# Performance work log

Measured on AMD Instinct MI355X. Metric: run time of the kernel, lower is better.

The kernel has to match this reference:

```python
import jax, jax.numpy as jnp
import numpy as np

N = 262144
DIM = 256
NUM_HEADS = 4
HEAD_DIM = DIM // NUM_HEADS
B = 4096
SCALE = HEAD_DIM ** (-0.5)
EPS = 1e-8


def setup_inputs() -> dict:
    key = jax.random.key(0)
    ks = jax.random.split(key, 7)
    x = jax.random.normal(ks[0], (N, DIM), dtype=jnp.float32)
    batch = jnp.sort(jax.random.randint(ks[1], (N,), 0, B)).astype(jnp.int64)
    query = jax.random.normal(ks[2], (NUM_HEADS, HEAD_DIM), dtype=jnp.float32)
    # nn.Linear default init scale ~ 1/sqrt(dim); keep exp() well-behaved
    key_w = jax.random.normal(ks[3], (DIM, DIM), dtype=jnp.float32) / np.sqrt(DIM)
    key_b = jax.random.normal(ks[4], (DIM,), dtype=jnp.float32) * 0.01
    value_w = jax.random.normal(ks[5], (DIM, DIM), dtype=jnp.float32) / np.sqrt(DIM)
    value_b = jax.random.normal(ks[6], (DIM,), dtype=jnp.float32) * 0.01
    return {"x": x, "batch": batch, "query": query, "key_w": key_w,
            "key_b": key_b, "value_w": value_w, "value_b": value_b}


def reference(x, batch, query, key_w, key_b, value_w, value_b):
    # k, v: [N, H, Hd]  (torch Linear: x @ W.T + b)
    k = (x @ key_w.T + key_b).reshape(N, NUM_HEADS, HEAD_DIM)
    v = (x @ value_w.T + value_b).reshape(N, NUM_HEADS, HEAD_DIM)
    # attn: [N, H] -- dot of learned per-head query with each node's key
    attn = jnp.einsum('hd,nhd->nh', query, k) * SCALE
    attn_exp = jnp.exp(attn)  # faithful: no max-subtraction in original
    # segment softmax denominator gathered back to nodes: [N, H]
    attn_sum = jax.ops.segment_sum(attn_exp, batch, num_segments=B)[batch]
    attn_norm = attn_exp / (attn_sum + EPS)
    # weighted values scatter-added per segment: [B, H, Hd]
    weighted = attn_norm[:, :, None] * v
    pooled = jax.ops.segment_sum(weighted, batch, num_segments=B)
    return pooled.reshape(B, DIM)
```

## Files before the change

### kernel.cpp

```cpp
#include <hip/hip_runtime.h>


constexpr int DIM = 256;
constexpr int NH  = 4;
constexpr int HD  = 64;
constexpr float SCL  = 0.125f;
constexpr float EPSV = 1e-8f;

constexpr int WS_QW   = 0;
constexpr int WS_QB   = 1024;
constexpr int WS_OFFS = 1088;
constexpr int WS_VWT  = 8192;

template<int CTRL>
__device__ __forceinline__ float dpp_ror_add(float v){
  int r = __builtin_amdgcn_update_dpp(0, __float_as_int(v), CTRL, 0xF, 0xF, false);
  return v + __int_as_float(r);
}
__device__ __forceinline__ float red32(float v){
  v = dpp_ror_add<0x121>(v);
  v = dpp_ror_add<0x122>(v);
  v = dpp_ror_add<0x124>(v);
  v = dpp_ror_add<0x128>(v);
  int r = __builtin_amdgcn_ds_swizzle(__float_as_int(v), 0x401F);
  return v + __int_as_float(r);
}

__global__ void prep_seg(const float* __restrict__ query,
                         const float* __restrict__ key_w,
                         const float* __restrict__ key_b,
                         const float* __restrict__ value_w,
                         const int* __restrict__ batch32,
                         float* __restrict__ ws,
                         int* __restrict__ offs,
                         int N, int B, int do_vwt){
  const int bid = blockIdx.x, tid = threadIdx.x;
  if (bid < 64){
    if (do_vwt){
      float4 v = *(const float4*)(value_w + (size_t)tid*DIM + 4*bid);
      ((float4*)(ws + WS_VWT))[bid*256 + tid] = v;
    }
  } else if (bid < 68){
    int t = (bid - 64)*256 + tid;
    int h = t >> 8, j = t & 255;
    float acc = 0.f;
    #pragma unroll 8
    for (int d = 0; d < HD; ++d)
      acc += query[h*HD+d] * key_w[(size_t)(h*HD+d)*DIM + j];
    ws[WS_QW + t] = acc;
    if (j == 0){
      float bb = 0.f;
      for (int d = 0; d < HD; ++d)
        bb += query[h*HD+d] * key_b[h*HD+d];
      ws[WS_QB + h] = bb;
    }
  } else {
    int i = (bid - 68)*256 + tid;
    if (i >= N) return;
    const bool is64 = (batch32[N-1] == 0);
    int v  = is64 ? batch32[2*i] : batch32[i];
    int vp = (i == 0) ? -1 : (is64 ? batch32[2*(i-1)] : batch32[i-1]);
    for (int b = vp + 1; b <= v; ++b) offs[b] = i;
    if (i == N-1)
      for (int b = v + 1; b <= B; ++b) offs[b] = N;
  }
}

__global__ __launch_bounds__(256, 4)
void attn_fused2(const float* __restrict__ x,
                 const int* __restrict__ offs,
                 const float* __restrict__ ws,
                 const float* __restrict__ value_b,
                 float* __restrict__ out){
  __shared__ __align__(16) float S_all[4][NH*DIM];
  __shared__ __align__(16) float Sfin[NH*DIM];
  __shared__ float sums_all[4][NH];
  __shared__ float invs[NH], wsums[NH];

  const int b   = blockIdx.x;
  const int tid = threadIdx.x;
  const int s = offs[b], e = offs[b+1];

  const int wave = tid >> 6, lane = tid & 63;
  const int half = lane >> 5, sl = lane & 31;
  const int sigma = wave * 2 + half;

  float qwr[NH][8];
  #pragma unroll
  for (int h = 0; h < NH; ++h){
    float4 a = *(const float4*)(ws + WS_QW + h*DIM + 4*sl);
    float4 c = *(const float4*)(ws + WS_QW + h*DIM + 128 + 4*sl);
    qwr[h][0]=a.x; qwr[h][1]=a.y; qwr[h][2]=a.z; qwr[h][3]=a.w;
    qwr[h][4]=c.x; qwr[h][5]=c.y; qwr[h][6]=c.z; qwr[h][7]=c.w;
  }
  float qb[NH];
  #pragma unroll
  for (int h = 0; h < NH; ++h) qb[h] = ws[WS_QB + h];

  float Sacc[NH][8];
  #pragma unroll
  for (int h = 0; h < NH; ++h)
    #pragma unroll
    for (int c = 0; c < 8; ++c) Sacc[h][c] = 0.f;
  float se[NH] = {0.f, 0.f, 0.f, 0.f};

  const float4* xr4 = (const float4*)x;
  const float4 Z = make_float4(0.f, 0.f, 0.f, 0.f);

  int n0 = s + sigma*2;
  bool v0 = n0 < e;
  bool v1 = n0 + 1 < e;
  float4 a0=Z, b0=Z, a1=Z, b1=Z;
  if (v0){ a0 = xr4[(size_t)n0*64 + sl];     b0 = xr4[(size_t)n0*64 + 32 + sl]; }
  if (v1){ a1 = xr4[(size_t)(n0+1)*64 + sl]; b1 = xr4[(size_t)(n0+1)*64 + 32 + sl]; }

  while (v0){
    const int nn = n0 + 16;
    const bool w0 = nn < e;
    const bool w1 = nn + 1 < e;
    float4 c0=Z, d0=Z, c1=Z, d1=Z;
    if (w0){ c0 = xr4[(size_t)nn*64 + sl];     d0 = xr4[(size_t)nn*64 + 32 + sl]; }
    if (w1){ c1 = xr4[(size_t)(nn+1)*64 + sl]; d1 = xr4[(size_t)(nn+1)*64 + 32 + sl]; }

    float xv0[8] = {a0.x,a0.y,a0.z,a0.w,b0.x,b0.y,b0.z,b0.w};
    float xv1[8] = {a1.x,a1.y,a1.z,a1.w,b1.x,b1.y,b1.z,b1.w};

    float p0[NH], p1[NH];
    #pragma unroll
    for (int h = 0; h < NH; ++h){
      float s0 = 0.f, s1 = 0.f;
      #pragma unroll
      for (int c = 0; c < 8; ++c){ s0 += qwr[h][c]*xv0[c]; s1 += qwr[h][c]*xv1[c]; }
      p0[h] = s0; p1[h] = s1;
    }
    #pragma unroll
    for (int h = 0; h < NH; ++h){
      p0[h] = red32(p0[h]);
      p1[h] = red32(p1[h]);
    }
    const float g1 = v1 ? 1.f : 0.f;
    #pragma unroll
    for (int h = 0; h < NH; ++h){
      float e0 = __expf((p0[h] + qb[h]) * SCL);
      float e1 = __expf((p1[h] + qb[h]) * SCL) * g1;
      se[h] += e0 + e1;
      #pragma unroll
      for (int c = 0; c < 8; ++c)
        Sacc[h][c] += e0*xv0[c] + e1*xv1[c];
    }
    n0 = nn; v0 = w0; v1 = w1;
    a0 = c0; b0 = d0; a1 = c1; b1 = d1;
  }

  #pragma unroll
  for (int h = 0; h < NH; ++h){
    se[h] += __shfl_xor(se[h], 32, 64);
    #pragma unroll
    for (int c = 0; c < 8; ++c) Sacc[h][c] += __shfl_xor(Sacc[h][c], 32, 64);
  }
  if (half == 0){
    #pragma unroll
    for (int h = 0; h < NH; ++h){
      float4 lo = make_float4(Sacc[h][0], Sacc[h][1], Sacc[h][2], Sacc[h][3]);
      float4 hi = make_float4(Sacc[h][4], Sacc[h][5], Sacc[h][6], Sacc[h][7]);
      *(float4*)&S_all[wave][h*DIM + 4*sl]       = lo;
      *(float4*)&S_all[wave][h*DIM + 128 + 4*sl] = hi;
    }
    if (sl == 0){
      #pragma unroll
      for (int h = 0; h < NH; ++h) sums_all[wave][h] = se[h];
    }
  }
  __syncthreads();

  #pragma unroll
  for (int k = 0; k < 4; ++k){
    const int idx = tid + k*256;
    Sfin[idx] = S_all[0][idx] + S_all[1][idx] + S_all[2][idx] + S_all[3][idx];
  }
  if (tid < NH){
    float tot = sums_all[0][tid] + sums_all[1][tid]
              + sums_all[2][tid] + sums_all[3][tid];
    float inv = 1.f / (tot + EPSV);
    invs[tid]  = inv;
    wsums[tid] = tot * inv;
  }
  __syncthreads();

  const int t = tid, h = t >> 6;
  const float4* vwt4 = (const float4*)(ws + WS_VWT);
  const float4* sp   = (const float4*)&Sfin[h*256];
  float acc = 0.f;
  #pragma unroll 8
  for (int jj = 0; jj < 64; ++jj){
    const float4 w4 = vwt4[jj*256 + t];
    const float4 s4 = sp[jj];
    acc += w4.x*s4.x + w4.y*s4.y + w4.z*s4.z + w4.w*s4.w;
  }
  out[(size_t)b*256 + t] = acc * invs[h] + wsums[h] * value_b[t];
}

__global__ __launch_bounds__(512, 4)
void attn_pool_fused(const float* __restrict__ x,
                     const int* __restrict__ offs,
                     const float* __restrict__ ws,
                     const float* __restrict__ value_w,
                     const float* __restrict__ value_b,
                     float* __restrict__ out){
  __shared__ __align__(16) float lds[8192 + 32 + 1024 + 512 + 8];
  float* S_all    = lds;
  float* sums_all = lds + 8192;

  const int b   = blockIdx.x;
  const int tid = threadIdx.x;
  const int seg_start = offs[b];
  const int seg_end   = offs[b+1];

  const int wave = tid >> 6, lane = tid & 63;
  const int half = lane >> 5, sl = lane & 31;
  const int sigma = wave * 2 + half;

  float qwr[NH][8];
  #pragma unroll
  for (int h = 0; h < NH; ++h){
    float4 a = *(const float4*)(ws + WS_QW + h*DIM + 4*sl);
    float4 c = *(const float4*)(ws + WS_QW + h*DIM + 128 + 4*sl);
    qwr[h][0]=a.x; qwr[h][1]=a.y; qwr[h][2]=a.z; qwr[h][3]=a.w;
    qwr[h][4]=c.x; qwr[h][5]=c.y; qwr[h][6]=c.z; qwr[h][7]=c.w;
  }
  float qb[NH];
  #pragma unroll
  for (int h = 0; h < NH; ++h) qb[h] = ws[WS_QB + h];

  float Sacc[NH][8];
  #pragma unroll
  for (int h = 0; h < NH; ++h)
    #pragma unroll
    for (int c = 0; c < 8; ++c) Sacc[h][c] = 0.f;
  float se[NH] = {0.f, 0.f, 0.f, 0.f};

  const float4* xr4 = (const float4*)x;
  const float4 Z = make_float4(0.f,0.f,0.f,0.f);

  int n0 = seg_start + sigma*2;
  bool v0 = n0 < seg_end;
  bool v1 = n0 + 1 < seg_end;
  float4 a0=Z, b0=Z, a1=Z, b1=Z;
  if (v0){ a0 = xr4[(size_t)n0*64 + sl];     b0 = xr4[(size_t)n0*64 + 32 + sl]; }
  if (v1){ a1 = xr4[(size_t)(n0+1)*64 + sl]; b1 = xr4[(size_t)(n0+1)*64 + 32 + sl]; }

  while (v0){
    const int nn = n0 + 32;
    const bool w0 = nn < seg_end;
    const bool w1 = nn + 1 < seg_end;
    float4 c0=Z, d0=Z, c1=Z, d1=Z;
    if (w0){ c0 = xr4[(size_t)nn*64 + sl];     d0 = xr4[(size_t)nn*64 + 32 + sl]; }
    if (w1){ c1 = xr4[(size_t)(nn+1)*64 + sl]; d1 = xr4[(size_t)(nn+1)*64 + 32 + sl]; }

    float xv0[8] = {a0.x,a0.y,a0.z,a0.w,b0.x,b0.y,b0.z,b0.w};
    float xv1[8] = {a1.x,a1.y,a1.z,a1.w,b1.x,b1.y,b1.z,b1.w};

    float p0[NH], p1[NH];
    #pragma unroll
    for (int h = 0; h < NH; ++h){
      float s0 = 0.f, s1 = 0.f;
      #pragma unroll
      for (int c = 0; c < 8; ++c){ s0 += qwr[h][c]*xv0[c]; s1 += qwr[h][c]*xv1[c]; }
      p0[h] = s0; p1[h] = s1;
    }
    #pragma unroll
    for (int m = 1; m < 32; m <<= 1){
      #pragma unroll
      for (int h = 0; h < NH; ++h){
        p0[h] += __shfl_xor(p0[h], m, 64);
        p1[h] += __shfl_xor(p1[h], m, 64);
      }
    }
    const float g1 = v1 ? 1.f : 0.f;
    #pragma unroll
    for (int h = 0; h < NH; ++h){
      float e0 = __expf((p0[h] + qb[h]) * SCL);
      float e1 = __expf((p1[h] + qb[h]) * SCL) * g1;
      se[h] += e0 + e1;
      #pragma unroll
      for (int c = 0; c < 8; ++c)
        Sacc[h][c] += e0*xv0[c] + e1*xv1[c];
    }
    n0 = nn; v0 = w0; v1 = w1;
    a0 = c0; b0 = d0; a1 = c1; b1 = d1;
  }

  #pragma unroll
  for (int h = 0; h < NH; ++h){
    se[h] += __shfl_xor(se[h], 32, 64);
    #pragma unroll
    for (int c = 0; c < 8; ++c) Sacc[h][c] += __shfl_xor(Sacc[h][c], 32, 64);
  }
  if (half == 0){
    #pragma unroll
    for (int h = 0; h < NH; ++h){
      float4 lo = make_float4(Sacc[h][0], Sacc[h][1], Sacc[h][2], Sacc[h][3]);
      float4 hi = make_float4(Sacc[h][4], Sacc[h][5], Sacc[h][6], Sacc[h][7]);
      *(float4*)&S_all[wave*1024 + h*DIM + 4*sl]       = lo;
      *(float4*)&S_all[wave*1024 + h*DIM + 128 + 4*sl] = hi;
    }
    if (sl == 0){
      #pragma unroll
      for (int h = 0; h < NH; ++h) sums_all[wave*4 + h] = se[h];
    }
  }
  __syncthreads();

  float* Sfin  = lds + 8224;
  float* invs  = lds + 9760;
  float* wsums = invs + 4;
  #pragma unroll
  for (int k = 0; k < 2; ++k){
    const int idx = tid + k*512;
    float sv = 0.f;
    #pragma unroll
    for (int w = 0; w < 8; ++w) sv += S_all[w*1024 + idx];
    Sfin[idx] = sv;
  }
  if (tid < NH){
    float tot = 0.f;
    #pragma unroll
    for (int w = 0; w < 8; ++w) tot += sums_all[w*4 + tid];
    float inv = 1.f / (tot + EPSV);
    invs[tid] = inv; wsums[tid] = tot * inv;
  }
  __syncthreads();

  float* ep2 = lds + 9248;
  const int t = tid & 255, part = tid >> 8;
  const int h2 = t >> 6;
  const float4* vrow = (const float4*)(value_w + (size_t)t * DIM) + part*32;
  const float4* sp   = (const float4*)&Sfin[h2*256] + part*32;
  float acc = 0.f;
  #pragma unroll
  for (int q = 0; q < 32; ++q){
    float4 r = vrow[q];
    float4 sv = sp[q];
    acc += r.x*sv.x + r.y*sv.y + r.z*sv.z + r.w*sv.w;
  }
  ep2[part*256 + t] = acc;
  __syncthreads();
  if (part == 0)
    out[(size_t)b * DIM + t] = (ep2[t] + ep2[256 + t]) * invs[h2] + wsums[h2] * value_b[t];
}

extern "C" void kernel_launch(void* const* d_in, const int* in_sizes, int n_in,
                              void* d_out, int out_size, void* d_ws, size_t ws_size,
                              hipStream_t stream){
  const float* x       = (const float*)d_in[0];
  const int*   batch   = (const int*)d_in[1];
  const float* query   = (const float*)d_in[2];
  const float* key_w   = (const float*)d_in[3];
  const float* key_b   = (const float*)d_in[4];
  const float* value_w = (const float*)d_in[5];
  const float* value_b = (const float*)d_in[6];
  float* ws  = (float*)d_ws;
  float* out = (float*)d_out;

  const int N = in_sizes[1];
  const int B = out_size / DIM;

  int* offs = (int*)(ws + WS_OFFS);

  const size_t need_vwt = ((size_t)WS_VWT + 65536) * sizeof(float);
  const int do_vwt = (ws_size >= need_vwt) ? 1 : 0;

  const int seg_blocks = (N + 255) / 256;
  prep_seg<<<68 + seg_blocks, 256, 0, stream>>>(query, key_w, key_b, value_w,
                                                batch, ws, offs, N, B, do_vwt);
  if (do_vwt)
    attn_fused2<<<B, 256, 0, stream>>>(x, offs, ws, value_b, out);
  else
    attn_pool_fused<<<B, 512, 0, stream>>>(x, offs, ws, value_w, value_b, out);
}
```

Measured before the change: 393.4 us.

## Stage segment rows through double-buffered LDS tiles with block-cooperative loads

The main attention-pooling kernel now loads each 16-row tile of x cooperatively into a double-buffered shared-memory tile, using fully coalesced float4 loads clamped at the segment end. While the current tile is being computed, the next tile is prefetched into registers. The shared buffer is reused afterwards for the per-wave partial sums. Occupancy is lowered to 3 blocks per CU, and every tile now costs a block-wide barrier, which adds sync overhead compared with the old per-wave register prefetch.

```diff
diff --git a/kernel.cpp b/kernel.cpp
--- a/kernel.cpp
+++ b/kernel.cpp
@@ -66,20 +66,20 @@
   }
 }
 
-__global__ __launch_bounds__(256, 4)
-void attn_fused2(const float* __restrict__ x,
-                 const int* __restrict__ offs,
-                 const float* __restrict__ ws,
-                 const float* __restrict__ value_b,
-                 float* __restrict__ out){
-  __shared__ __align__(16) float S_all[4][NH*DIM];
-  __shared__ __align__(16) float Sfin[NH*DIM];
+__global__ __launch_bounds__(256, 3)
+void attn_tile(const float* __restrict__ x,
+               const int* __restrict__ offs,
+               const float* __restrict__ ws,
+               const float* __restrict__ value_b,
+               float* __restrict__ out){
+  __shared__ __align__(16) float lds[8192];
   __shared__ float sums_all[4][NH];
   __shared__ float invs[NH], wsums[NH];
 
   const int b   = blockIdx.x;
   const int tid = threadIdx.x;
   const int s = offs[b], e = offs[b+1];
+  const int len = e - s;
 
   const int wave = tid >> 6, lane = tid & 63;
   const int half = lane >> 5, sl = lane & 31;
@@ -105,52 +105,83 @@
   float se[NH] = {0.f, 0.f, 0.f, 0.f};
 
   const float4* xr4 = (const float4*)x;
-  const float4 Z = make_float4(0.f, 0.f, 0.f, 0.f);
-
-  int n0 = s + sigma*2;
-  bool v0 = n0 < e;
-  bool v1 = n0 + 1 < e;
-  float4 a0=Z, b0=Z, a1=Z, b1=Z;
-  if (v0){ a0 = xr4[(size_t)n0*64 + sl];     b0 = xr4[(size_t)n0*64 + 32 + sl]; }
-  if (v1){ a1 = xr4[(size_t)(n0+1)*64 + sl]; b1 = xr4[(size_t)(n0+1)*64 + 32 + sl]; }
-
-  while (v0){
-    const int nn = n0 + 16;
-    const bool w0 = nn < e;
-    const bool w1 = nn + 1 < e;
-    float4 c0=Z, d0=Z, c1=Z, d1=Z;
-    if (w0){ c0 = xr4[(size_t)nn*64 + sl];     d0 = xr4[(size_t)nn*64 + 32 + sl]; }
-    if (w1){ c1 = xr4[(size_t)(nn+1)*64 + sl]; d1 = xr4[(size_t)(nn+1)*64 + 32 + sl]; }
-
-    float xv0[8] = {a0.x,a0.y,a0.z,a0.w,b0.x,b0.y,b0.z,b0.w};
-    float xv1[8] = {a1.x,a1.y,a1.z,a1.w,b1.x,b1.y,b1.z,b1.w};
-
-    float p0[NH], p1[NH];
-    #pragma unroll
-    for (int h = 0; h < NH; ++h){
-      float s0 = 0.f, s1 = 0.f;
-      #pragma unroll
-      for (int c = 0; c < 8; ++c){ s0 += qwr[h][c]*xv0[c]; s1 += qwr[h][c]*xv1[c]; }
-      p0[h] = s0; p1[h] = s1;
-    }
-    #pragma unroll
-    for (int h = 0; h < NH; ++h){
-      p0[h] = red32(p0[h]);
-      p1[h] = red32(p1[h]);
-    }
-    const float g1 = v1 ? 1.f : 0.f;
-    #pragma unroll
-    for (int h = 0; h < NH; ++h){
-      float e0 = __expf((p0[h] + qb[h]) * SCL);
-      float e1 = __expf((p1[h] + qb[h]) * SCL) * g1;
-      se[h] += e0 + e1;
-      #pragma unroll
-      for (int c = 0; c < 8; ++c)
-        Sacc[h][c] += e0*xv0[c] + e1*xv1[c];
-    }
-    n0 = nn; v0 = w0; v1 = w1;
-    a0 = c0; b0 = d0; a1 = c1; b1 = d1;
-  }
+  float4* lbuf4 = (float4*)lds;
+
+  if (len > 0){
+    const int ntiles = (len + 15) >> 4;
+    const long gmax = (long)e * 64 - 1;
+
+    {
+      float4 r0[4];
+      #pragma unroll
+      for (int j = 0; j < 4; ++j){
+        long gi = (long)s*64 + tid + j*256;
+        gi = gi < gmax ? gi : gmax;
+        r0[j] = xr4[gi];
+      }
+      #pragma unroll
+      for (int j = 0; j < 4; ++j) lbuf4[tid + j*256] = r0[j];
+    }
+    __syncthreads();
+
+    int cur = 0;
+    for (int k = 0; k < ntiles; ++k){
+      float4 rn[4];
+      const bool more = (k + 1 < ntiles);
+      if (more){
+        const long tb = (long)(s + (k+1)*16) * 64;
+        #pragma unroll
+        for (int j = 0; j < 4; ++j){
+          long gi = tb + tid + j*256;
+          gi = gi < gmax ? gi : gmax;
+          rn[j] = xr4[gi];
+        }
+      }
+
+      const float* base = lds + cur*4096;
+      const int gr0 = s + k*16 + 2*sigma;
+      float4 a0 = *(const float4*)(base + (2*sigma)*256 + 4*sl);
+      float4 b0 = *(const float4*)(base + (2*sigma)*256 + 128 + 4*sl);
+      float4 a1 = *(const float4*)(base + (2*sigma+1)*256 + 4*sl);
+      float4 b1 = *(const float4*)(base + (2*sigma+1)*256 + 128 + 4*sl);
+
+      float xv0[8] = {a0.x,a0.y,a0.z,a0.w,b0.x,b0.y,b0.z,b0.w};
+      float xv1[8] = {a1.x,a1.y,a1.z,a1.w,b1.x,b1.y,b1.z,b1.w};
+
+      float p0[NH], p1[NH];
+      #pragma unroll
+      for (int h = 0; h < NH; ++h){
+        float s0 = 0.f, s1 = 0.f;
+        #pragma unroll
+        for (int c = 0; c < 8; ++c){ s0 += qwr[h][c]*xv0[c]; s1 += qwr[h][c]*xv1[c]; }
+        p0[h] = s0; p1[h] = s1;
+      }
+      #pragma unroll
+      for (int h = 0; h < NH; ++h){
+        p0[h] = red32(p0[h]);
+        p1[h] = red32(p1[h]);
+      }
+      const float g0 = (gr0     < e) ? 1.f : 0.f;
+      const float g1 = (gr0 + 1 < e) ? 1.f : 0.f;
+      #pragma unroll
+      for (int h = 0; h < NH; ++h){
+        float e0 = __expf((p0[h] + qb[h]) * SCL) * g0;
+        float e1 = __expf((p1[h] + qb[h]) * SCL) * g1;
+        se[h] += e0 + e1;
+        #pragma unroll
+        for (int c = 0; c < 8; ++c)
+          Sacc[h][c] += e0*xv0[c] + e1*xv1[c];
+      }
+
+      if (more){
+        #pragma unroll
+        for (int j = 0; j < 4; ++j) lbuf4[(cur^1)*1024 + tid + j*256] = rn[j];
+      }
+      __syncthreads();
+      cur ^= 1;
+    }
+  }
+  __syncthreads();
 
   #pragma unroll
   for (int h = 0; h < NH; ++h){
@@ -158,13 +189,15 @@
     #pragma unroll
     for (int c = 0; c < 8; ++c) Sacc[h][c] += __shfl_xor(Sacc[h][c], 32, 64);
   }
+  float* S_all = lds;
+  float* Sfin  = lds + 4096;
   if (half == 0){
     #pragma unroll
     for (int h = 0; h < NH; ++h){
       float4 lo = make_float4(Sacc[h][0], Sacc[h][1], Sacc[h][2], Sacc[h][3]);
       float4 hi = make_float4(Sacc[h][4], Sacc[h][5], Sacc[h][6], Sacc[h][7]);
-      *(float4*)&S_all[wave][h*DIM + 4*sl]       = lo;
-      *(float4*)&S_all[wave][h*DIM + 128 + 4*sl] = hi;
+      *(float4*)&S_all[wave*1024 + h*DIM + 4*sl]       = lo;
+      *(float4*)&S_all[wave*1024 + h*DIM + 128 + 4*sl] = hi;
     }
     if (sl == 0){
       #pragma unroll
@@ -176,7 +209,8 @@
   #pragma unroll
   for (int k = 0; k < 4; ++k){
     const int idx = tid + k*256;
-    Sfin[idx] = S_all[0][idx] + S_all[1][idx] + S_all[2][idx] + S_all[3][idx];
+    Sfin[idx] = S_all[0*1024 + idx] + S_all[1*1024 + idx]
+              + S_all[2*1024 + idx] + S_all[3*1024 + idx];
   }
   if (tid < NH){
     float tot = sums_all[0][tid] + sums_all[1][tid]
@@ -374,7 +408,7 @@
   prep_seg<<<68 + seg_blocks, 256, 0, stream>>>(query, key_w, key_b, value_w,
                                                 batch, ws, offs, N, B, do_vwt);
   if (do_vwt)
-    attn_fused2<<<B, 256, 0, stream>>>(x, offs, ws, value_b, out);
+    attn_tile<<<B, 256, 0, stream>>>(x, offs, ws, value_b, out);
   else
     attn_pool_fused<<<B, 512, 0, stream>>>(x, offs, ws, value_w, value_b, out);
 }
```

New measurement: 442.6 us. 12.5% more time.

## Process eight segments per block to amortize value-weight projection loads

Applied to the files above, without the earlier changes.

Each block now handles eight consecutive segments with 512 threads. It accumulates per-segment weighted x sums in LDS, then runs one shared pass over the transposed value weights that serves all eight segments, splitting the 64-step reduction across two thread halves. This is meant to cut the repeated global reads of the 256 KB value-weight matrix per segment and the per-block launch overhead. In exchange the grid shrinks from 4096 to 512 blocks, there are many more __syncthreads, and segments within a block are processed serially, which can hurt load balance and occupancy.

```diff
diff --git a/kernel.cpp b/kernel.cpp
--- a/kernel.cpp
+++ b/kernel.cpp
@@ -4,6 +4,7 @@
 constexpr int DIM = 256;
 constexpr int NH  = 4;
 constexpr int HD  = 64;
+constexpr int G   = 8;
 constexpr float SCL  = 0.125f;
 constexpr float EPSV = 1e-8f;
 
@@ -66,21 +67,19 @@
   }
 }
 
-__global__ __launch_bounds__(256, 4)
-void attn_fused2(const float* __restrict__ x,
-                 const int* __restrict__ offs,
-                 const float* __restrict__ ws,
-                 const float* __restrict__ value_b,
-                 float* __restrict__ out){
-  __shared__ __align__(16) float S_all[4][NH*DIM];
-  __shared__ __align__(16) float Sfin[NH*DIM];
-  __shared__ float sums_all[4][NH];
-  __shared__ float invs[NH], wsums[NH];
-
-  const int b   = blockIdx.x;
+__global__ __launch_bounds__(512, 4)
+void attn_g8(const float* __restrict__ x,
+             const int* __restrict__ offs,
+             const float* __restrict__ ws,
+             const float* __restrict__ value_b,
+             float* __restrict__ out){
+  __shared__ __align__(16) float S_all[8][1024];
+  __shared__ __align__(16) float Sfin[G][1024];
+  __shared__ float sums_all[8][NH];
+  __shared__ float invs[G][NH], wsums[G][NH];
+
+  const int b0  = blockIdx.x * G;
   const int tid = threadIdx.x;
-  const int s = offs[b], e = offs[b+1];
-
   const int wave = tid >> 6, lane = tid & 63;
   const int half = lane >> 5, sl = lane & 31;
   const int sigma = wave * 2 + half;
@@ -97,107 +96,131 @@
   #pragma unroll
   for (int h = 0; h < NH; ++h) qb[h] = ws[WS_QB + h];
 
-  float Sacc[NH][8];
-  #pragma unroll
-  for (int h = 0; h < NH; ++h)
-    #pragma unroll
-    for (int c = 0; c < 8; ++c) Sacc[h][c] = 0.f;
-  float se[NH] = {0.f, 0.f, 0.f, 0.f};
-
   const float4* xr4 = (const float4*)x;
   const float4 Z = make_float4(0.f, 0.f, 0.f, 0.f);
 
-  int n0 = s + sigma*2;
-  bool v0 = n0 < e;
-  bool v1 = n0 + 1 < e;
-  float4 a0=Z, b0=Z, a1=Z, b1=Z;
-  if (v0){ a0 = xr4[(size_t)n0*64 + sl];     b0 = xr4[(size_t)n0*64 + 32 + sl]; }
-  if (v1){ a1 = xr4[(size_t)(n0+1)*64 + sl]; b1 = xr4[(size_t)(n0+1)*64 + 32 + sl]; }
-
-  while (v0){
-    const int nn = n0 + 16;
-    const bool w0 = nn < e;
-    const bool w1 = nn + 1 < e;
-    float4 c0=Z, d0=Z, c1=Z, d1=Z;
-    if (w0){ c0 = xr4[(size_t)nn*64 + sl];     d0 = xr4[(size_t)nn*64 + 32 + sl]; }
-    if (w1){ c1 = xr4[(size_t)(nn+1)*64 + sl]; d1 = xr4[(size_t)(nn+1)*64 + 32 + sl]; }
-
-    float xv0[8] = {a0.x,a0.y,a0.z,a0.w,b0.x,b0.y,b0.z,b0.w};
-    float xv1[8] = {a1.x,a1.y,a1.z,a1.w,b1.x,b1.y,b1.z,b1.w};
-
-    float p0[NH], p1[NH];
+  for (int g = 0; g < G; ++g){
+    const int s = offs[b0 + g], e = offs[b0 + g + 1];
+
+    float Sacc[NH][8];
+    #pragma unroll
+    for (int h = 0; h < NH; ++h)
+      #pragma unroll
+      for (int c = 0; c < 8; ++c) Sacc[h][c] = 0.f;
+    float se[NH] = {0.f, 0.f, 0.f, 0.f};
+
+    int n0 = s + sigma*2;
+    bool v0 = n0 < e;
+    bool v1 = n0 + 1 < e;
+    float4 la0=Z, lb0=Z, la1=Z, lb1=Z;
+    if (v0){ la0 = xr4[(size_t)n0*64 + sl];     lb0 = xr4[(size_t)n0*64 + 32 + sl]; }
+    if (v1){ la1 = xr4[(size_t)(n0+1)*64 + sl]; lb1 = xr4[(size_t)(n0+1)*64 + 32 + sl]; }
+
+    while (v0){
+      const int nn = n0 + 32;
+      const bool w0 = nn < e;
+      const bool w1 = nn + 1 < e;
+      float4 nc0=Z, nd0=Z, nc1=Z, nd1=Z;
+      if (w0){ nc0 = xr4[(size_t)nn*64 + sl];     nd0 = xr4[(size_t)nn*64 + 32 + sl]; }
+      if (w1){ nc1 = xr4[(size_t)(nn+1)*64 + sl]; nd1 = xr4[(size_t)(nn+1)*64 + 32 + sl]; }
+
+      float xv0[8] = {la0.x,la0.y,la0.z,la0.w,lb0.x,lb0.y,lb0.z,lb0.w};
+      float xv1[8] = {la1.x,la1.y,la1.z,la1.w,lb1.x,lb1.y,lb1.z,lb1.w};
+
+      float p0[NH], p1[NH];
+      #pragma unroll
+      for (int h = 0; h < NH; ++h){
+        float s0 = 0.f, s1 = 0.f;
+        #pragma unroll
+        for (int c = 0; c < 8; ++c){ s0 += qwr[h][c]*xv0[c]; s1 += qwr[h][c]*xv1[c]; }
+        p0[h] = s0; p1[h] = s1;
+      }
+      #pragma unroll
+      for (int h = 0; h < NH; ++h){
+        p0[h] = red32(p0[h]);
+        p1[h] = red32(p1[h]);
+      }
+      const float g1 = v1 ? 1.f : 0.f;
+      #pragma unroll
+      for (int h = 0; h < NH; ++h){
+        float e0 = __expf((p0[h] + qb[h]) * SCL);
+        float e1 = __expf((p1[h] + qb[h]) * SCL) * g1;
+        se[h] += e0 + e1;
+        #pragma unroll
+        for (int c = 0; c < 8; ++c)
+          Sacc[h][c] += e0*xv0[c] + e1*xv1[c];
+      }
+      n0 = nn; v0 = w0; v1 = w1;
+      la0 = nc0; lb0 = nd0; la1 = nc1; lb1 = nd1;
+    }
+
     #pragma unroll
     for (int h = 0; h < NH; ++h){
-      float s0 = 0.f, s1 = 0.f;
-      #pragma unroll
-      for (int c = 0; c < 8; ++c){ s0 += qwr[h][c]*xv0[c]; s1 += qwr[h][c]*xv1[c]; }
-      p0[h] = s0; p1[h] = s1;
-    }
-    #pragma unroll
-    for (int h = 0; h < NH; ++h){
-      p0[h] = red32(p0[h]);
-      p1[h] = red32(p1[h]);
-    }
-    const float g1 = v1 ? 1.f : 0.f;
-    #pragma unroll
-    for (int h = 0; h < NH; ++h){
-      float e0 = __expf((p0[h] + qb[h]) * SCL);
-      float e1 = __expf((p1[h] + qb[h]) * SCL) * g1;
-      se[h] += e0 + e1;
-      #pragma unroll
-      for (int c = 0; c < 8; ++c)
-        Sacc[h][c] += e0*xv0[c] + e1*xv1[c];
-    }
-    n0 = nn; v0 = w0; v1 = w1;
-    a0 = c0; b0 = d0; a1 = c1; b1 = d1;
-  }
-
-  #pragma unroll
-  for (int h = 0; h < NH; ++h){
-    se[h] += __shfl_xor(se[h], 32, 64);
-    #pragma unroll
-    for (int c = 0; c < 8; ++c) Sacc[h][c] += __shfl_xor(Sacc[h][c], 32, 64);
-  }
-  if (half == 0){
-    #pragma unroll
-    for (int h = 0; h < NH; ++h){
-      float4 lo = make_float4(Sacc[h][0], Sacc[h][1], Sacc[h][2], Sacc[h][3]);
-      float4 hi = make_float4(Sacc[h][4], Sacc[h][5], Sacc[h][6], Sacc[h][7]);
-      *(float4*)&S_all[wave][h*DIM + 4*sl]       = lo;
-      *(float4*)&S_all[wave][h*DIM + 128 + 4*sl] = hi;
-    }
-    if (sl == 0){
-      #pragma unroll
-      for (int h = 0; h < NH; ++h) sums_all[wave][h] = se[h];
-    }
-  }
+      se[h] += __shfl_xor(se[h], 32, 64);
+      #pragma unroll
+      for (int c = 0; c < 8; ++c) Sacc[h][c] += __shfl_xor(Sacc[h][c], 32, 64);
+    }
+    if (half == 0){
+      #pragma unroll
+      for (int h = 0; h < NH; ++h){
+        float4 lo = make_float4(Sacc[h][0], Sacc[h][1], Sacc[h][2], Sacc[h][3]);
+        float4 hi = make_float4(Sacc[h][4], Sacc[h][5], Sacc[h][6], Sacc[h][7]);
+        *(float4*)&S_all[wave][h*DIM + 4*sl]       = lo;
+        *(float4*)&S_all[wave][h*DIM + 128 + 4*sl] = hi;
+      }
+      if (sl == 0){
+        #pragma unroll
+        for (int h = 0; h < NH; ++h) sums_all[wave][h] = se[h];
+      }
+    }
+    __syncthreads();
+
+    #pragma unroll
+    for (int k2 = 0; k2 < 2; ++k2){
+      const int idx = tid + k2*512;
+      float sv = 0.f;
+      #pragma unroll
+      for (int w = 0; w < 8; ++w) sv += S_all[w][idx];
+      Sfin[g][idx] = sv;
+    }
+    if (tid < NH){
+      float tot = 0.f;
+      #pragma unroll
+      for (int w = 0; w < 8; ++w) tot += sums_all[w][tid];
+      float inv = 1.f / (tot + EPSV);
+      invs[g][tid]  = inv;
+      wsums[g][tid] = tot * inv;
+    }
+    __syncthreads();
+  }
+
+  const int t = tid & 255, part = tid >> 8, h = t >> 6;
+  const float4* vwt4 = (const float4*)(ws + WS_VWT);
+  float acc[G];
+  #pragma unroll
+  for (int g = 0; g < G; ++g) acc[g] = 0.f;
+
+  #pragma unroll 4
+  for (int jj = part*32; jj < part*32 + 32; ++jj){
+    const float4 w4 = vwt4[jj*256 + t];
+    #pragma unroll
+    for (int g = 0; g < G; ++g){
+      const float4 s4 = *(const float4*)&Sfin[g][h*256 + 4*jj];
+      acc[g] += w4.x*s4.x + w4.y*s4.y + w4.z*s4.z + w4.w*s4.w;
+    }
+  }
+  float* ep = &S_all[0][0];
+  #pragma unroll
+  for (int g = 0; g < G; ++g) ep[(part*G + g)*256 + t] = acc[g];
   __syncthreads();
-
-  #pragma unroll
-  for (int k = 0; k < 4; ++k){
-    const int idx = tid + k*256;
-    Sfin[idx] = S_all[0][idx] + S_all[1][idx] + S_all[2][idx] + S_all[3][idx];
-  }
-  if (tid < NH){
-    float tot = sums_all[0][tid] + sums_all[1][tid]
-              + sums_all[2][tid] + sums_all[3][tid];
-    float inv = 1.f / (tot + EPSV);
-    invs[tid]  = inv;
-    wsums[tid] = tot * inv;
-  }
-  __syncthreads();
-
-  const int t = tid, h = t >> 6;
-  const float4* vwt4 = (const float4*)(ws + WS_VWT);
-  const float4* sp   = (const float4*)&Sfin[h*256];
-  float acc = 0.f;
-  #pragma unroll 8
-  for (int jj = 0; jj < 64; ++jj){
-    const float4 w4 = vwt4[jj*256 + t];
-    const float4 s4 = sp[jj];
-    acc += w4.x*s4.x + w4.y*s4.y + w4.z*s4.z + w4.w*s4.w;
-  }
-  out[(size_t)b*256 + t] = acc * invs[h] + wsums[h] * value_b[t];
+  if (part == 0){
+    const float vb = value_b[t];
+    #pragma unroll
+    for (int g = 0; g < G; ++g){
+      out[(size_t)(b0 + g)*256 + t] =
+          (ep[g*256 + t] + ep[(G + g)*256 + t]) * invs[g][h] + wsums[g][h] * vb;
+    }
+  }
 }
 
 __global__ __launch_bounds__(512, 4)
@@ -373,8 +396,8 @@
   const int seg_blocks = (N + 255) / 256;
   prep_seg<<<68 + seg_blocks, 256, 0, stream>>>(query, key_w, key_b, value_w,
                                                 batch, ws, offs, N, B, do_vwt);
-  if (do_vwt)
-    attn_fused2<<<B, 256, 0, stream>>>(x, offs, ws, value_b, out);
+  if (do_vwt && (B % G) == 0)
+    attn_g8<<<B / G, 512, 0, stream>>>(x, offs, ws, value_b, out);
   else
     attn_pool_fused<<<B, 512, 0, stream>>>(x, offs, ws, value_w, value_b, out);
 }
```

After: 402.2 us. +2.3%, slower.

## Merge prep and attention pooling into one cooperative kernel with grid sync

Applied to the files above, without the earlier changes.

Replaces the two-launch path (prep_seg, then attn_fused2) with a single cooperative kernel. Blocks first build the transposed value weights and the query-key projection, then use a grid-wide sync before streaming x per segment. Segment offsets come from a per-block binary search over batch instead of a separate offsets pass. Each block handles four segments so the value-weight matmul epilogue reuses each weight load four times, at the cost of fewer blocks (B/4) and a grid barrier that requires all blocks to be co-resident.

```diff
diff --git a/kernel.cpp b/kernel.cpp
--- a/kernel.cpp
+++ b/kernel.cpp
@@ -1,4 +1,7 @@
 #include <hip/hip_runtime.h>
+#include <hip/hip_cooperative_groups.h>
+
+namespace cg = cooperative_groups;
 
 
 constexpr int DIM = 256;
@@ -24,6 +27,191 @@
   v = dpp_ror_add<0x128>(v);
   int r = __builtin_amdgcn_ds_swizzle(__float_as_int(v), 0x401F);
   return v + __int_as_float(r);
+}
+
+__global__ __launch_bounds__(256, 4)
+void attn_coop(const float* __restrict__ x,
+               const int* __restrict__ batch32,
+               const float* __restrict__ query,
+               const float* __restrict__ key_w,
+               const float* __restrict__ key_b,
+               const float* __restrict__ value_w,
+               float* __restrict__ ws,
+               const float* __restrict__ value_b,
+               float* __restrict__ out,
+               int N, int B){
+  constexpr int G4 = 4;
+  __shared__ __align__(16) float S_all[4][1024];
+  __shared__ __align__(16) float Sfin[G4][1024];
+  __shared__ float sums_all[4][NH];
+  __shared__ float invs[G4][NH], wsums[G4][NH];
+  __shared__ int offsL[G4 + 1];
+
+  const int bid = blockIdx.x, tid = threadIdx.x;
+  const int b0  = bid * G4;
+
+  if (bid < 64){
+    float4 v = *(const float4*)(value_w + (size_t)tid*DIM + 4*bid);
+    ((float4*)(ws + WS_VWT))[bid*256 + tid] = v;
+  } else if (bid < 68){
+    int t = (bid - 64)*256 + tid;
+    int h = t >> 8, j = t & 255;
+    float acc = 0.f;
+    #pragma unroll 8
+    for (int d = 0; d < HD; ++d)
+      acc += query[h*HD+d] * key_w[(size_t)(h*HD+d)*DIM + j];
+    ws[WS_QW + t] = acc;
+    if (j == 0){
+      float bb = 0.f;
+      for (int d = 0; d < HD; ++d)
+        bb += query[h*HD+d] * key_b[h*HD+d];
+      ws[WS_QB + h] = bb;
+    }
+  }
+
+  const bool is64 = (batch32[N-1] == 0);
+  if (tid <= G4){
+    const int target = b0 + tid;
+    int lo = 0, hi = N;
+    while (lo < hi){
+      const int mid = (lo + hi) >> 1;
+      const int v = is64 ? batch32[2*(size_t)mid] : batch32[mid];
+      if (v < target) lo = mid + 1; else hi = mid;
+    }
+    offsL[tid] = lo;
+  }
+
+  __threadfence();
+  cg::this_grid().sync();
+  __threadfence();
+  __syncthreads();
+
+  const int wave = tid >> 6, lane = tid & 63;
+  const int half = lane >> 5, sl = lane & 31;
+  const int sigma = wave * 2 + half;
+
+  float qwr[NH][8];
+  #pragma unroll
+  for (int h = 0; h < NH; ++h){
+    float4 a = *(const float4*)(ws + WS_QW + h*DIM + 4*sl);
+    float4 c = *(const float4*)(ws + WS_QW + h*DIM + 128 + 4*sl);
+    qwr[h][0]=a.x; qwr[h][1]=a.y; qwr[h][2]=a.z; qwr[h][3]=a.w;
+    qwr[h][4]=c.x; qwr[h][5]=c.y; qwr[h][6]=c.z; qwr[h][7]=c.w;
+  }
+  float qb[NH];
+  #pragma unroll
+  for (int h = 0; h < NH; ++h) qb[h] = ws[WS_QB + h];
+
+  const float4* xr4 = (const float4*)x;
+  const float4 Z = make_float4(0.f, 0.f, 0.f, 0.f);
+
+  for (int g = 0; g < G4; ++g){
+    const int s = offsL[g], e = offsL[g+1];
+
+    float Sacc[NH][8];
+    #pragma unroll
+    for (int h = 0; h < NH; ++h)
+      #pragma unroll
+      for (int c = 0; c < 8; ++c) Sacc[h][c] = 0.f;
+    float se[NH] = {0.f, 0.f, 0.f, 0.f};
+
+    int n0 = s + sigma*2;
+    bool v0 = n0 < e;
+    bool v1 = n0 + 1 < e;
+    float4 a0=Z, b0v=Z, a1=Z, b1=Z;
+    if (v0){ a0 = xr4[(size_t)n0*64 + sl];     b0v = xr4[(size_t)n0*64 + 32 + sl]; }
+    if (v1){ a1 = xr4[(size_t)(n0+1)*64 + sl]; b1  = xr4[(size_t)(n0+1)*64 + 32 + sl]; }
+
+    while (v0){
+      const int nn = n0 + 16;
+      const bool w0 = nn < e;
+      const bool w1 = nn + 1 < e;
+      float4 c0=Z, d0=Z, c1=Z, d1=Z;
+      if (w0){ c0 = xr4[(size_t)nn*64 + sl];     d0 = xr4[(size_t)nn*64 + 32 + sl]; }
+      if (w1){ c1 = xr4[(size_t)(nn+1)*64 + sl]; d1 = xr4[(size_t)(nn+1)*64 + 32 + sl]; }
+
+      float xv0[8] = {a0.x,a0.y,a0.z,a0.w,b0v.x,b0v.y,b0v.z,b0v.w};
+      float xv1[8] = {a1.x,a1.y,a1.z,a1.w,b1.x,b1.y,b1.z,b1.w};
+
+      float p0[NH], p1[NH];
+      #pragma unroll
+      for (int h = 0; h < NH; ++h){
+        float s0 = 0.f, s1 = 0.f;
+        #pragma unroll
+        for (int c = 0; c < 8; ++c){ s0 += qwr[h][c]*xv0[c]; s1 += qwr[h][c]*xv1[c]; }
+        p0[h] = s0; p1[h] = s1;
+      }
+      #pragma unroll
+      for (int h = 0; h < NH; ++h){
+        p0[h] = red32(p0[h]);
+        p1[h] = red32(p1[h]);
+      }
+      const float g1 = v1 ? 1.f : 0.f;
+      #pragma unroll
+      for (int h = 0; h < NH; ++h){
+        float e0 = __expf((p0[h] + qb[h]) * SCL);
+        float e1 = __expf((p1[h] + qb[h]) * SCL) * g1;
+        se[h] += e0 + e1;
+        #pragma unroll
+        for (int c = 0; c < 8; ++c)
+          Sacc[h][c] += e0*xv0[c] + e1*xv1[c];
+      }
+      n0 = nn; v0 = w0; v1 = w1;
+      a0 = c0; b0v = d0; a1 = c1; b1 = d1;
+    }
+
+    #pragma unroll
+    for (int h = 0; h < NH; ++h){
+      se[h] += __shfl_xor(se[h], 32, 64);
+      #pragma unroll
+      for (int c = 0; c < 8; ++c) Sacc[h][c] += __shfl_xor(Sacc[h][c], 32, 64);
+    }
+    if (half == 0){
+      #pragma unroll
+      for (int h = 0; h < NH; ++h){
+        float4 lo = make_float4(Sacc[h][0], Sacc[h][1], Sacc[h][2], Sacc[h][3]);
+        float4 hi = make_float4(Sacc[h][4], Sacc[h][5], Sacc[h][6], Sacc[h][7]);
+        *(float4*)&S_all[wave][h*DIM + 4*sl]       = lo;
+        *(float4*)&S_all[wave][h*DIM + 128 + 4*sl] = hi;
+      }
+      if (sl == 0){
+        #pragma unroll
+        for (int h = 0; h < NH; ++h) sums_all[wave][h] = se[h];
+      }
+    }
+    __syncthreads();
+
+    #pragma unroll
+    for (int k = 0; k < 4; ++k){
+      const int idx = tid + k*256;
+      Sfin[g][idx] = S_all[0][idx] + S_all[1][idx] + S_all[2][idx] + S_all[3][idx];
+    }
+    if (tid < NH){
+      float tot = sums_all[0][tid] + sums_all[1][tid]
+                + sums_all[2][tid] + sums_all[3][tid];
+      float inv = 1.f / (tot + EPSV);
+      invs[g][tid]  = inv;
+      wsums[g][tid] = tot * inv;
+    }
+    __syncthreads();
+  }
+
+  const int t = tid, h = t >> 6;
+  const float4* vwt4 = (const float4*)(ws + WS_VWT);
+  float acc[G4] = {0.f, 0.f, 0.f, 0.f};
+  #pragma unroll 8
+  for (int jj = 0; jj < 64; ++jj){
+    const float4 w4 = vwt4[jj*256 + t];
+    #pragma unroll
+    for (int g = 0; g < G4; ++g){
+      const float4 s4 = *(const float4*)&Sfin[g][h*256 + 4*jj];
+      acc[g] += w4.x*s4.x + w4.y*s4.y + w4.z*s4.z + w4.w*s4.w;
+    }
+  }
+  const float vb = value_b[t];
+  #pragma unroll
+  for (int g = 0; g < G4; ++g)
+    out[(size_t)(b0 + g)*256 + t] = acc[g]*invs[g][h] + wsums[g][h]*vb;
 }
 
 __global__ void prep_seg(const float* __restrict__ query,
@@ -362,19 +550,33 @@
   float* ws  = (float*)d_ws;
   float* out = (float*)d_out;
 
-  const int N = in_sizes[1];
-  const int B = out_size / DIM;
-
-  int* offs = (int*)(ws + WS_OFFS);
+  int N = in_sizes[1];
+  int B = out_size / DIM;
 
   const size_t need_vwt = ((size_t)WS_VWT + 65536) * sizeof(float);
   const int do_vwt = (ws_size >= need_vwt) ? 1 : 0;
 
-  const int seg_blocks = (N + 255) / 256;
-  prep_seg<<<68 + seg_blocks, 256, 0, stream>>>(query, key_w, key_b, value_w,
-                                                batch, ws, offs, N, B, do_vwt);
-  if (do_vwt)
-    attn_fused2<<<B, 256, 0, stream>>>(x, offs, ws, value_b, out);
-  else
-    attn_pool_fused<<<B, 512, 0, stream>>>(x, offs, ws, value_w, value_b, out);
-}
+  bool coop_done = false;
+  if (do_vwt && (B % 4) == 0 && (B / 4) <= 1024){
+    const float* xa = x;  const int* ba = batch;  const float* qa = query;
+    const float* kwa = key_w;  const float* kba = key_b;  const float* vwa = value_w;
+    float* wsa = ws;  const float* vba = value_b;  float* oa = out;
+    int Na = N, Ba = B;
+    void* args[] = {&xa, &ba, &qa, &kwa, &kba, &vwa, &wsa, &vba, &oa, &Na, &Ba};
+    hipError_t st = hipLaunchCooperativeKernel((const void*)attn_coop,
+                                               dim3(B / 4), dim3(256),
+                                               args, 0, stream);
+    coop_done = (st == hipSuccess);
+  }
+
+  if (!coop_done){
+    int* offs = (int*)(ws + WS_OFFS);
+    const int seg_blocks = (N + 255) / 256;
+    prep_seg<<<68 + seg_blocks, 256, 0, stream>>>(query, key_w, key_b, value_w,
+                                                  batch, ws, offs, N, B, do_vwt);
+    if (do_vwt)
+      attn_fused2<<<B, 256, 0, stream>>>(x, offs, ws, value_b, out);
+    else
+      attn_pool_fused<<<B, 512, 0, stream>>>(x, offs, ws, value_w, value_b, out);
+  }
+}
```

After: 651.4 us. 1.66x slower.
